# Performance work log

Hardware: AMD Instinct MI355X
Metric: run time of the kernel (lower is better)

Reference implementation:

```python
import jax, jax.numpy as jnp
import numpy as np

N_NODE = 100000
N_EDGE = 1600000
D_FEAT = 64
DEPTH = 10
BASEALPHA = 1.0
JAC_A, JAC_B, JAC_L, JAC_R = 1.0, 1.0, -1.0, 1.0


def setup_inputs() -> dict:
    key = jax.random.key(0)
    k1, k2, k3 = jax.random.split(key, 3)
    x = jax.random.normal(k1, (N_NODE, D_FEAT), dtype=jnp.float32)
    edge_attr = jnp.ones((N_EDGE,), dtype=jnp.float32)
    alpha_params = jnp.ones((DEPTH + 1,), dtype=jnp.float32)  # torch init min(1/alpha,1)=1.0
    edge_index = jax.random.randint(k2, (2, N_EDGE), 0, N_NODE, dtype=jnp.int64)
    return {"x": x, "edge_attr": edge_attr, "alpha_params": alpha_params, "edge_index": edge_index}


def _forward(x, edge_attr, alpha_params, edge_index):
    n = x.shape[0]
    row, col = edge_index[0], edge_index[1]
    # gcn normalization: deg from out-degree of row; deg<0.5 -> +1
    deg = jax.ops.segment_sum(jnp.ones_like(edge_attr), row, num_segments=n)
    deg = jnp.where(deg < 0.5, deg + 1.0, deg)
    dinv = deg ** -0.5
    val = dinv[row] * edge_attr * dinv[col]  # [E]

    def spmm(y):  # adj @ y, COO with duplicate-summing (== coalesce)
        return jax.ops.segment_sum(val[:, None] * y[col], row, num_segments=n)

    alphas = BASEALPHA * jnp.tanh(alpha_params)  # [DEPTH+1]
    a, b, l, r = JAC_A, JAC_B, JAC_L, JAC_R

    xs = [x]
    # L = 1
    coef1 = (a - b) / 2 - (a + b + 2) / 2 * (l + r) / (r - l)
    coef2 = (a + b + 2) / (r - l)
    xs.append(alphas[0] * coef1 * x + alphas[0] * coef2 * spmm(x))
    # L >= 2 three-term recurrence
    for L in range(2, DEPTH + 1):
        coef_l = 2 * L * (L + a + b) * (2 * L - 2 + a + b)
        coef_lm1_1 = (2 * L + a + b - 1) * (2 * L + a + b) * (2 * L + a + b - 2)
        coef_lm1_2 = (2 * L + a + b - 1) * (a ** 2 - b ** 2)
        coef_lm2 = 2 * (L - 1 + a) * (L - 1 + b) * (2 * L + a + b)
        tmp1 = alphas[L - 1] * (coef_lm1_1 / coef_l)
        tmp2 = alphas[L - 1] * (coef_lm1_2 / coef_l)
        tmp3 = alphas[L - 1] * alphas[L - 2] * (coef_lm2 / coef_l)
        tmp1_2 = tmp1 * (2 / (r - l))
        tmp2_2 = tmp1 * ((r + l) / (r - l)) + tmp2
        nx = tmp1_2 * spmm(xs[-1]) - tmp2_2 * xs[-1] - tmp3 * xs[-2]
        xs.append(nx)
    return jnp.stack(xs, axis=1)  # [N, DEPTH+1, D]


def reference(x, edge_attr, alpha_params, edge_index):
    return _forward(x, edge_attr, alpha_params, edge_index)
```

## Files before the change

kernel.cpp:

```cpp
#include <hip/hip_runtime.h>

#define NNODE 100000
#define NEDGE 1600000
#define DFEAT 64
#define DEPTH 10
#define STRIDE ((DEPTH + 1) * DFEAT)
#define SCAN_BLK 256

typedef float float4v __attribute__((ext_vector_type(4)));
typedef unsigned short ushort8v __attribute__((ext_vector_type(8)));

__device__ inline float bf16_to_f32(unsigned short u) {
    return __uint_as_float(((unsigned int)u) << 16);
}
__device__ inline unsigned short f32_to_bf16_rne(float f) {
    unsigned int u = __float_as_uint(f);
    u += 0x7FFFu + ((u >> 16) & 1u);
    return (unsigned short)(u >> 16);
}


__global__ void hist_kernel(const int* __restrict__ ei, int* __restrict__ counts, int E) {
    int e = blockIdx.x * blockDim.x + threadIdx.x;
    if (e < E) atomicAdd(&counts[ei[e]], 1);
}

__global__ void scan1_kernel(const int* __restrict__ counts, int* __restrict__ blocksums, int n) {
    __shared__ int sh[SCAN_BLK];
    int t = threadIdx.x;
    int i = blockIdx.x * SCAN_BLK + t;
    sh[t] = (i < n) ? counts[i] : 0;
    __syncthreads();
    for (int off = SCAN_BLK / 2; off > 0; off >>= 1) {
        if (t < off) sh[t] += sh[t + off];
        __syncthreads();
    }
    if (t == 0) blocksums[blockIdx.x] = sh[0];
}

__global__ void scan2_kernel(const int* __restrict__ blocksums, int* __restrict__ blockoffs,
                             int* __restrict__ rowptr, int nb, int n) {
    __shared__ int sh[512];
    int t = threadIdx.x;
    int v = (t < nb) ? blocksums[t] : 0;
    sh[t] = v;
    __syncthreads();
    for (int off = 1; off < 512; off <<= 1) {
        int o = (t >= off) ? sh[t - off] : 0;
        __syncthreads();
        sh[t] += o;
        __syncthreads();
    }
    if (t < nb) blockoffs[t] = sh[t] - v;
    if (t == nb - 1) rowptr[n] = sh[t];
}

__global__ void scan3_kernel(const int* __restrict__ counts, const int* __restrict__ blockoffs,
                             int* __restrict__ rowptr, int* __restrict__ woff,
                             float* __restrict__ dinv, int n) {
    __shared__ int sh[SCAN_BLK];
    int t = threadIdx.x;
    int i = blockIdx.x * SCAN_BLK + t;
    int v = (i < n) ? counts[i] : 0;
    sh[t] = v;
    __syncthreads();
    for (int off = 1; off < SCAN_BLK; off <<= 1) {
        int o = (t >= off) ? sh[t - off] : 0;
        __syncthreads();
        sh[t] += o;
        __syncthreads();
    }
    if (i < n) {
        int excl = sh[t] - v + blockoffs[blockIdx.x];
        rowptr[i] = excl;
        woff[i] = excl;
        float d = (float)v;
        if (d < 0.5f) d += 1.0f;
        dinv[i] = rsqrtf(d);
    }
}

__global__ void scatter_kernel(const int* __restrict__ ei, const float* __restrict__ ea,
                               const float* __restrict__ dinv, int* __restrict__ woff,
                               int2* __restrict__ cvpack, int E) {
    int e = blockIdx.x * blockDim.x + threadIdx.x;
    if (e >= E) return;
    int r = ei[e];
    int c = ei[E + e];
    int pos = atomicAdd(&woff[r], 1);
    float v = dinv[r] * ea[e] * dinv[c];
    cvpack[pos] = make_int2(c, __float_as_int(v));
}

__global__ void coef_kernel(const float* __restrict__ alpha_params, float* __restrict__ coefs) {
    if (threadIdx.x != 0 || blockIdx.x != 0) return;
    const float a = 1.0f, b = 1.0f, l = -1.0f, r = 1.0f, basealpha = 1.0f;
    float alphas[DEPTH + 1];
    for (int i = 0; i <= DEPTH; ++i) alphas[i] = basealpha * tanhf(alpha_params[i]);
    float coef1 = (a - b) * 0.5f - (a + b + 2.0f) * 0.5f * (l + r) / (r - l);
    float coef2 = (a + b + 2.0f) / (r - l);
    coefs[3 * 1 + 0] = alphas[0] * coef2;
    coefs[3 * 1 + 1] = alphas[0] * coef1;
    coefs[3 * 1 + 2] = 0.0f;
    for (int L = 2; L <= DEPTH; ++L) {
        float Lf = (float)L;
        float coef_l = 2.0f * Lf * (Lf + a + b) * (2.0f * Lf - 2.0f + a + b);
        float coef_lm1_1 = (2.0f * Lf + a + b - 1.0f) * (2.0f * Lf + a + b) * (2.0f * Lf + a + b - 2.0f);
        float coef_lm1_2 = (2.0f * Lf + a + b - 1.0f) * (a * a - b * b);
        float coef_lm2 = 2.0f * (Lf - 1.0f + a) * (Lf - 1.0f + b) * (2.0f * Lf + a + b);
        float tmp1 = alphas[L - 1] * (coef_lm1_1 / coef_l);
        float tmp2 = alphas[L - 1] * (coef_lm1_2 / coef_l);
        float tmp3 = alphas[L - 1] * alphas[L - 2] * (coef_lm2 / coef_l);
        float tmp1_2 = tmp1 * (2.0f / (r - l));
        float tmp2_2 = tmp1 * ((r + l) / (r - l)) + tmp2;
        coefs[3 * L + 0] = tmp1_2;
        coefs[3 * L + 1] = -tmp2_2;
        coefs[3 * L + 2] = -tmp3;
    }
}

__global__ void copyx_kernel(const float* __restrict__ x, float* __restrict__ out,
                             unsigned short* __restrict__ xb16, int n) {
    int i = blockIdx.x * blockDim.x + threadIdx.x;
    if (i >= n * 16) return;
    int node = i >> 4;
    int q = i & 15;
    float4v v = ((const float4v*)x)[i];
    __builtin_nontemporal_store(v, (float4v*)(out + (size_t)node * STRIDE) + q);
    ushort4 b;
    b.x = f32_to_bf16_rne(v.x); b.y = f32_to_bf16_rne(v.y);
    b.z = f32_to_bf16_rne(v.z); b.w = f32_to_bf16_rne(v.w);
    ((ushort4*)xb16)[i] = b;
}

__global__ void spmm_kernel(const int* __restrict__ rowptr, const int2* __restrict__ cvpack,
                            const float* __restrict__ coefs,
                            const unsigned short* __restrict__ gsrc,
                            const unsigned short* __restrict__ p2src,
                            unsigned short* __restrict__ cur,
                            float* __restrict__ out, int n, int L) {
    int gid = blockIdx.x * blockDim.x + threadIdx.x;
    int node = gid >> 6;
    if (node >= n) return;
    int lane = threadIdx.x & 63;
    int g = lane >> 3;
    int f = lane & 7;
    int s = rowptr[node];
    int e_end = rowptr[node + 1];

    float acc[8];
#pragma unroll
    for (int j = 0; j < 8; ++j) acc[j] = 0.0f;

    for (int base = s; base < e_end; base += 16) {
        int e0 = base + g;
        int e1 = base + 8 + g;
        bool b0 = e0 < e_end, b1 = e1 < e_end;
        int2 p0 = b0 ? cvpack[e0] : make_int2(0, 0);
        int2 p1i = b1 ? cvpack[e1] : make_int2(0, 0);
        float v0 = __int_as_float(p0.y);
        float v1 = __int_as_float(p1i.y);
        ushort8v q0 = ((const ushort8v*)(gsrc + (size_t)p0.x * DFEAT))[f];
        ushort8v q1 = ((const ushort8v*)(gsrc + (size_t)p1i.x * DFEAT))[f];
#pragma unroll
        for (int j = 0; j < 8; ++j) {
            acc[j] += v0 * bf16_to_f32(q0[j]);
            acc[j] += v1 * bf16_to_f32(q1[j]);
        }
    }
#pragma unroll
    for (int j = 0; j < 8; ++j) {
        acc[j] += __shfl_xor(acc[j], 8, 64);
        acc[j] += __shfl_xor(acc[j], 16, 64);
        acc[j] += __shfl_xor(acc[j], 32, 64);
    }

    if (g == 0) {
        float cA = coefs[3 * L + 0];
        float cB = coefs[3 * L + 1];
        float cC = coefs[3 * L + 2];
        size_t nb = (size_t)node * DFEAT;
        ushort8v p1b = ((const ushort8v*)(gsrc + nb))[f];
        ushort8v p2b = ((const ushort8v*)(p2src + nb))[f];
        float r[8];
        ushort8v rb;
#pragma unroll
        for (int j = 0; j < 8; ++j) {
            r[j] = cA * acc[j] + cB * bf16_to_f32(p1b[j]) + cC * bf16_to_f32(p2b[j]);
            rb[j] = f32_to_bf16_rne(r[j]);
        }
        ((ushort8v*)(cur + nb))[f] = rb;
        float4v lo = {r[0], r[1], r[2], r[3]};
        float4v hi = {r[4], r[5], r[6], r[7]};
        float4v* obase = (float4v*)(out + (size_t)node * STRIDE + (size_t)L * DFEAT);
        __builtin_nontemporal_store(lo, obase + 2 * f);
        __builtin_nontemporal_store(hi, obase + 2 * f + 1);
    }
}

extern "C" void kernel_launch(void* const* d_in, const int* in_sizes, int n_in,
                              void* d_out, int out_size, void* d_ws, size_t ws_size,
                              hipStream_t stream) {
    const float* x = (const float*)d_in[0];
    const float* ea = (const float*)d_in[1];
    const float* alpha = (const float*)d_in[2];
    const int* ei = (const int*)d_in[3];
    float* out = (float*)d_out;
    int n = in_sizes[0] / DFEAT;
    int E = in_sizes[1];
    int nb = (n + SCAN_BLK - 1) / SCAN_BLK;

    char* ws = (char*)d_ws;
    size_t off = 0;
    auto alloc = [&](size_t bytes) -> void* {
        void* p = ws + off;
        off += (bytes + 255) & ~(size_t)255;
        return p;
    };
    int* counts = (int*)alloc((size_t)n * 4);
    int* rowptr = (int*)alloc((size_t)(n + 1) * 4);
    int* woff = (int*)alloc((size_t)n * 4);
    float* dinv = (float*)alloc((size_t)n * 4);
    int2* cvpack = (int2*)alloc((size_t)E * 8);
    float* coefs = (float*)alloc(3 * (DEPTH + 1) * 4);
    int* blocksums = (int*)alloc((size_t)nb * 4);
    int* blockoffs = (int*)alloc((size_t)nb * 4);
    unsigned short* xbA = (unsigned short*)alloc((size_t)n * DFEAT * 2);
    unsigned short* xbB = (unsigned short*)alloc((size_t)n * DFEAT * 2);
    unsigned short* xbC = (unsigned short*)alloc((size_t)n * DFEAT * 2);

    hipMemsetAsync(counts, 0, (size_t)n * 4, stream);
    hist_kernel<<<(E + 255) / 256, 256, 0, stream>>>(ei, counts, E);
    scan1_kernel<<<nb, SCAN_BLK, 0, stream>>>(counts, blocksums, n);
    scan2_kernel<<<1, 512, 0, stream>>>(blocksums, blockoffs, rowptr, nb, n);
    scan3_kernel<<<nb, SCAN_BLK, 0, stream>>>(counts, blockoffs, rowptr, woff, dinv, n);
    scatter_kernel<<<(E + 255) / 256, 256, 0, stream>>>(ei, ea, dinv, woff, cvpack, E);
    coef_kernel<<<1, 64, 0, stream>>>(alpha, coefs);
    copyx_kernel<<<(n * 16 + 255) / 256, 256, 0, stream>>>(x, out, xbA, n);

    int spmm_blocks = (int)(((size_t)n * 64 + 255) / 256);
    unsigned short* bufs[3] = {xbA, xbB, xbC};
    for (int L = 1; L <= DEPTH; ++L) {
        unsigned short* cur = bufs[L % 3];
        const unsigned short* gsrc = bufs[(L - 1) % 3];
        const unsigned short* p2src = bufs[(L + 1) % 3];
        spmm_kernel<<<spmm_blocks, 256, 0, stream>>>(rowptr, cvpack, coefs, gsrc, p2src, cur, out, n, L);
    }
}
```

Before: 648.0 us.

## Fuse all SpMM recurrence layers into one cooperative kernel with grid syncs

Replaces the ten per-layer SpMM launches with a single cooperative kernel of 1024 blocks. Each block processes a contiguous range of nodes, one wave per node, and steps through all layers, rotating the three bf16 buffers and calling grid.sync between layers. This removes per-launch overhead and the tail gaps between launches. In exchange it caps the grid at 1024 blocks of 4 waves, which may lower the memory-level parallelism available for the gather-heavy SpMM, and it adds the cost of a grid-wide barrier per layer.

```diff
diff --git a/kernel.cpp b/kernel.cpp
--- a/kernel.cpp
+++ b/kernel.cpp
@@ -1,4 +1,7 @@
 #include <hip/hip_runtime.h>
+#include <hip/hip_cooperative_groups.h>
+
+namespace cg = cooperative_groups;
 
 #define NNODE 100000
 #define NEDGE 1600000
@@ -6,6 +9,7 @@
 #define DEPTH 10
 #define STRIDE ((DEPTH + 1) * DFEAT)
 #define SCAN_BLK 256
+#define COOP_BLOCKS 1024
 
 typedef float float4v __attribute__((ext_vector_type(4)));
 typedef unsigned short ushort8v __attribute__((ext_vector_type(8)));
@@ -133,68 +137,85 @@
     ((ushort4*)xb16)[i] = b;
 }
 
-__global__ void spmm_kernel(const int* __restrict__ rowptr, const int2* __restrict__ cvpack,
-                            const float* __restrict__ coefs,
-                            const unsigned short* __restrict__ gsrc,
-                            const unsigned short* __restrict__ p2src,
-                            unsigned short* __restrict__ cur,
-                            float* __restrict__ out, int n, int L) {
-    int gid = blockIdx.x * blockDim.x + threadIdx.x;
-    int node = gid >> 6;
-    if (node >= n) return;
+__global__ void spmm_all_kernel(const int* __restrict__ rowptr, const int2* __restrict__ cvpack,
+                                const float* __restrict__ coefs,
+                                unsigned short* xbA, unsigned short* xbB, unsigned short* xbC,
+                                float* __restrict__ out, int n, int npb) {
+    cg::grid_group grid = cg::this_grid();
     int lane = threadIdx.x & 63;
+    int w = threadIdx.x >> 6;
     int g = lane >> 3;
     int f = lane & 7;
-    int s = rowptr[node];
-    int e_end = rowptr[node + 1];
-
-    float acc[8];
-#pragma unroll
-    for (int j = 0; j < 8; ++j) acc[j] = 0.0f;
-
-    for (int base = s; base < e_end; base += 16) {
-        int e0 = base + g;
-        int e1 = base + 8 + g;
-        bool b0 = e0 < e_end, b1 = e1 < e_end;
-        int2 p0 = b0 ? cvpack[e0] : make_int2(0, 0);
-        int2 p1i = b1 ? cvpack[e1] : make_int2(0, 0);
-        float v0 = __int_as_float(p0.y);
-        float v1 = __int_as_float(p1i.y);
-        ushort8v q0 = ((const ushort8v*)(gsrc + (size_t)p0.x * DFEAT))[f];
-        ushort8v q1 = ((const ushort8v*)(gsrc + (size_t)p1i.x * DFEAT))[f];
-#pragma unroll
-        for (int j = 0; j < 8; ++j) {
-            acc[j] += v0 * bf16_to_f32(q0[j]);
-            acc[j] += v1 * bf16_to_f32(q1[j]);
-        }
-    }
-#pragma unroll
-    for (int j = 0; j < 8; ++j) {
-        acc[j] += __shfl_xor(acc[j], 8, 64);
-        acc[j] += __shfl_xor(acc[j], 16, 64);
-        acc[j] += __shfl_xor(acc[j], 32, 64);
-    }
-
-    if (g == 0) {
+    int nodeBase = blockIdx.x * npb;
+    int nodeEnd = nodeBase + npb;
+    if (nodeEnd > n) nodeEnd = n;
+
+    unsigned short* gsrc = xbA;
+    unsigned short* p2src = xbC;
+    unsigned short* cur = xbB;
+
+    for (int L = 1; L <= DEPTH; ++L) {
         float cA = coefs[3 * L + 0];
         float cB = coefs[3 * L + 1];
         float cC = coefs[3 * L + 2];
-        size_t nb = (size_t)node * DFEAT;
-        ushort8v p1b = ((const ushort8v*)(gsrc + nb))[f];
-        ushort8v p2b = ((const ushort8v*)(p2src + nb))[f];
-        float r[8];
-        ushort8v rb;
-#pragma unroll
-        for (int j = 0; j < 8; ++j) {
-            r[j] = cA * acc[j] + cB * bf16_to_f32(p1b[j]) + cC * bf16_to_f32(p2b[j]);
-            rb[j] = f32_to_bf16_rne(r[j]);
+
+        for (int node = nodeBase + w; node < nodeEnd; node += 4) {
+            int s = rowptr[node];
+            int e_end = rowptr[node + 1];
+
+            float acc[8];
+#pragma unroll
+            for (int j = 0; j < 8; ++j) acc[j] = 0.0f;
+
+            for (int base = s; base < e_end; base += 16) {
+                int e0 = base + g;
+                int e1 = base + 8 + g;
+                bool b0 = e0 < e_end, b1 = e1 < e_end;
+                int2 p0 = b0 ? cvpack[e0] : make_int2(0, 0);
+                int2 p1i = b1 ? cvpack[e1] : make_int2(0, 0);
+                float v0 = __int_as_float(p0.y);
+                float v1 = __int_as_float(p1i.y);
+                ushort8v q0 = ((const ushort8v*)(gsrc + (size_t)p0.x * DFEAT))[f];
+                ushort8v q1 = ((const ushort8v*)(gsrc + (size_t)p1i.x * DFEAT))[f];
+#pragma unroll
+                for (int j = 0; j < 8; ++j) {
+                    acc[j] += v0 * bf16_to_f32(q0[j]);
+                    acc[j] += v1 * bf16_to_f32(q1[j]);
+                }
+            }
+#pragma unroll
+            for (int j = 0; j < 8; ++j) {
+                acc[j] += __shfl_xor(acc[j], 8, 64);
+                acc[j] += __shfl_xor(acc[j], 16, 64);
+                acc[j] += __shfl_xor(acc[j], 32, 64);
+            }
+
+            if (g == 0) {
+                size_t nb = (size_t)node * DFEAT;
+                ushort8v p1b = ((const ushort8v*)(gsrc + nb))[f];
+                ushort8v p2b = ((const ushort8v*)(p2src + nb))[f];
+                float r[8];
+                ushort8v rb;
+#pragma unroll
+                for (int j = 0; j < 8; ++j) {
+                    r[j] = cA * acc[j] + cB * bf16_to_f32(p1b[j]) + cC * bf16_to_f32(p2b[j]);
+                    rb[j] = f32_to_bf16_rne(r[j]);
+                }
+                ((ushort8v*)(cur + nb))[f] = rb;
+                float4v lo = {r[0], r[1], r[2], r[3]};
+                float4v hi = {r[4], r[5], r[6], r[7]};
+                float4v* obase = (float4v*)(out + (size_t)node * STRIDE + (size_t)L * DFEAT);
+                __builtin_nontemporal_store(lo, obase + 2 * f);
+                __builtin_nontemporal_store(hi, obase + 2 * f + 1);
+            }
         }
-        ((ushort8v*)(cur + nb))[f] = rb;
-        float4v lo = {r[0], r[1], r[2], r[3]};
-        float4v hi = {r[4], r[5], r[6], r[7]};
-        float4v* obase = (float4v*)(out + (size_t)node * STRIDE + (size_t)L * DFEAT);
-        __builtin_nontemporal_store(lo, obase + 2 * f);
-        __builtin_nontemporal_store(hi, obase + 2 * f + 1);
+
+        unsigned short* t = p2src;
+        p2src = gsrc;
+        gsrc = cur;
+        cur = t;
+
+        grid.sync();
     }
 }
 
@@ -238,12 +259,10 @@
     coef_kernel<<<1, 64, 0, stream>>>(alpha, coefs);
     copyx_kernel<<<(n * 16 + 255) / 256, 256, 0, stream>>>(x, out, xbA, n);
 
-    int spmm_blocks = (int)(((size_t)n * 64 + 255) / 256);
-    unsigned short* bufs[3] = {xbA, xbB, xbC};
-    for (int L = 1; L <= DEPTH; ++L) {
-        unsigned short* cur = bufs[L % 3];
-        const unsigned short* gsrc = bufs[(L - 1) % 3];
-        const unsigned short* p2src = bufs[(L + 1) % 3];
-        spmm_kernel<<<spmm_blocks, 256, 0, stream>>>(rowptr, cvpack, coefs, gsrc, p2src, cur, out, n, L);
-    }
-}
+    int npb = (n + COOP_BLOCKS - 1) / COOP_BLOCKS;
+    void* kargs[] = {(void*)&rowptr, (void*)&cvpack, (void*)&coefs,
+                     (void*)&xbA, (void*)&xbB, (void*)&xbC,
+                     (void*)&out, (void*)&n, (void*)&npb};
+    hipLaunchCooperativeKernel((void*)spmm_all_kernel, dim3(COOP_BLOCKS), dim3(256),
+                               kargs, 0, stream);
+}
```

New measurement: 2.114 ms. 3.26x slower.
